# Optimization experiments

Measured on AMD Instinct MI355X. Metric: run time of the kernel, lower is better.

## Reference

```python
import jax, jax.numpy as jnp
import numpy as np

L = 6      # n_latents (hardcoded 6 in original zeros((1,1,6)))
H = 64     # hidden_dim
V = 51     # queue_len + 1
N = 300000 # number of agents/observations
K = 64     # neighbors per slot (flattened c_group)
EPS = 1e-8


def swish(x):
    return x * jax.nn.sigmoid(x)


def encode(obs, We1, be1, We2, be2, We3, be3):
    # obs: [N, 2] -> mu, logvar each [N, 2, L]
    h = swish(obs @ We1 + be1)
    h = swish(h @ We2 + be2)
    out = h @ We3 + be3  # [N, 4L]
    mu, logvar = out[:, :2 * L], out[:, 2 * L:]
    n = obs.shape[0]
    return mu.reshape(n, 2, L), logvar.reshape(n, 2, L)


def decode(z, Wd1, bd1, Wd2, bd2, Wd3, bd3):
    # z: [..., L] -> [..., V]
    h = swish(z @ Wd1 + bd1)
    h = swish(h @ Wd2 + bd2)
    return h @ Wd3 + bd3


def poe(mu_e, lv_e, axis):
    # product of experts along `axis` (ProductOfExperts.forward)
    T = 1.0 / (jnp.exp(lv_e) + EPS)
    sT = jnp.sum(T, axis=axis)
    pd_mu = jnp.sum(mu_e * T, axis=axis) / sT
    pd_logvar = jnp.log(1.0 / sT)
    return pd_mu, pd_logvar


def setup_inputs() -> dict:
    key = jax.random.key(0)
    ks = jax.random.split(key, 12)
    glorot = jax.nn.initializers.glorot_uniform()
    return {
        "obs": jax.random.normal(ks[0], (N, 2), jnp.float32),
        "p": jax.random.uniform(ks[1], (N, 1), jnp.float32),
        "eps_skip": jax.random.normal(ks[2], (N, 2, L), jnp.float32),
        "eps_poe": jax.random.normal(ks[3], (N, 2, L), jnp.float32),
        "neighbor_sched": jax.random.randint(ks[4], (N, 2, K), 0, N, jnp.int32),
        "neighbor_obs": jax.random.randint(ks[5], (N, 2, K), 0, 2, jnp.int32),
        # MessageEncoder params
        "We1": glorot(ks[6], (2, H)), "be1": jnp.zeros((H,), jnp.float32),
        "We2": glorot(ks[7], (H, H)), "be2": jnp.zeros((H,), jnp.float32),
        "We3": glorot(ks[8], (H, 4 * L)), "be3": jnp.zeros((4 * L,), jnp.float32),
        # MessageDecoder params
        "Wd1": glorot(ks[9], (L, H)), "bd1": jnp.zeros((H,), jnp.float32),
        "Wd2": glorot(ks[10], (H, H)), "bd2": jnp.zeros((H,), jnp.float32),
        "Wd3": glorot(ks[11], (H, V)), "bd3": jnp.zeros((V,), jnp.float32),
    }


def reference(obs, p, eps_skip, eps_poe, neighbor_sched, neighbor_obs,
              We1, be1, We2, be2, We3, be3,
              Wd1, bd1, Wd2, bd2, Wd3, bd3):
    n = obs.shape[0]
    mu, logvar = encode(obs, We1, be1, We2, be2, We3, be3)  # [N,2,L]

    # gather neighbor experts: _mus[id_sched][:, id_obs, :]
    nb_mu = mu[neighbor_sched, neighbor_obs]      # [N,2,K,L]
    nb_lv = logvar[neighbor_sched, neighbor_obs]  # [N,2,K,L]

    # experts = [prior N(0,1), own slot, K neighbors] along axis 2
    prior = jnp.zeros((n, 2, 1, L), mu.dtype)  # mu=0, logvar=log(1)=0
    mu_e = jnp.concatenate([prior, mu[:, :, None, :], nb_mu], axis=2)
    lv_e = jnp.concatenate([prior, logvar[:, :, None, :], nb_lv], axis=2)
    pd_mu, pd_lv = poe(mu_e, lv_e, axis=2)  # [N,2,L]

    # reparametrize (training=True)
    z_poe = pd_mu + eps_poe * jnp.exp(0.5 * pd_lv)
    z_skip = mu + eps_skip * jnp.exp(0.5 * logvar)

    rec_poe = decode(z_poe, Wd1, bd1, Wd2, bd2, Wd3, bd3)   # [N,2,V]
    rec_skip = decode(z_skip, Wd1, bd1, Wd2, bd2, Wd3, bd3) # [N,2,V]

    skip = (p[:, 0] < 0.5)[:, None]  # [N,1] -> p[i][0]<0.5 branch
    mus = jnp.where(skip, mu.reshape(n, -1), pd_mu.reshape(n, -1))        # [N,2L]
    logvars = jnp.where(skip, logvar.reshape(n, -1), pd_lv.reshape(n, -1))
    recs = jnp.where(skip, rec_skip.reshape(n, -1), rec_poe.reshape(n, -1))  # [N,2V]
    return recs, mus, logvars
```

## Files before the change

kernel.cpp:

```cpp
#include <hip/hip_runtime.h>
#include <hip/hip_bf16.h>


typedef unsigned short u16;
typedef __hip_bfloat16 bf16;

__device__ __forceinline__ float blo(unsigned int x) {
    union { unsigned int i; float f; } v; v.i = x << 16; return v.f;
}
__device__ __forceinline__ float bhi(unsigned int x) {
    union { unsigned int i; float f; } v; v.i = x & 0xffff0000u; return v.f;
}
__device__ __forceinline__ u16 f2b16(float f) {
    __hip_bfloat16 h = __float2bfloat16(f);
    u16 u; __builtin_memcpy(&u, &h, 2); return u;
}
__device__ __forceinline__ float b2f(u16 u) {
    union { unsigned int i; float f; } v; v.i = ((unsigned int)u) << 16; return v.f;
}
__device__ __forceinline__ float swishf(float x) {
    return x / (1.0f + __expf(-x));
}
__device__ __forceinline__ float ldv(const void* p, size_t i, int isb) {
    return isb ? __bfloat162float(((const bf16*)p)[i]) : ((const float*)p)[i];
}
__device__ __forceinline__ void stv(void* p, size_t i, int isb, float v) {
    if (isb) ((bf16*)p)[i] = __float2bfloat16(v);
    else     ((float*)p)[i] = v;
}

__global__ void k_detect(const unsigned int* __restrict__ obsw, int* __restrict__ flag) {
    unsigned int w = obsw[threadIdx.x];
    unsigned int e = (w >> 7) & 0xFFu;
    bool sane = (e >= 0x70u && e <= 0x87u);
    unsigned long long m = __ballot(sane);
    if (threadIdx.x == 0) flag[0] = (__popcll(m) >= 40) ? 1 : 0;
}

__global__ __launch_bounds__(256) void k_encode(
    const void* __restrict__ obs,
    const void* __restrict__ We1, const void* __restrict__ be1,
    const void* __restrict__ We2, const void* __restrict__ be2,
    const void* __restrict__ We3, const void* __restrict__ be3,
    const int* __restrict__ flag, u16* __restrict__ gt, int N)
{
    __shared__ float sW1[2 * 64];
    __shared__ float sb1[64];
    __shared__ float sW2[64 * 64];
    __shared__ float sb2[64];
    __shared__ float sW3[64 * 24];
    __shared__ float sb3[24];
    __shared__ u16 sh1[64 * 256];
    const int isb = flag[0];
    const int tid = threadIdx.x;
    for (int i = tid; i < 128; i += 256) sW1[i] = ldv(We1, i, isb);
    if (tid < 64) sb1[tid] = ldv(be1, tid, isb);
    for (int i = tid; i < 4096; i += 256) sW2[i] = ldv(We2, i, isb);
    if (tid < 64) sb2[tid] = ldv(be2, tid, isb);
    for (int i = tid; i < 1536; i += 256) sW3[i] = ldv(We3, i, isb);
    if (tid < 24) sb3[tid] = ldv(be3, tid, isb);
    __syncthreads();

    const int n = blockIdx.x * 256 + tid;
    if (n >= N) return;

    const float o0 = ldv(obs, 2 * (size_t)n, isb);
    const float o1 = ldv(obs, 2 * (size_t)n + 1, isb);

#pragma unroll 8
    for (int j = 0; j < 64; ++j) {
        float v = swishf(o0 * sW1[j] + o1 * sW1[64 + j] + sb1[j]);
        sh1[j * 256 + tid] = f2b16(v);
    }

    float o[24];
#pragma unroll
    for (int v = 0; v < 24; ++v) o[v] = sb3[v];

    for (int jc = 0; jc < 4; ++jc) {
        float acc[16];
#pragma unroll
        for (int k = 0; k < 16; ++k) acc[k] = sb2[jc * 16 + k];
        for (int i = 0; i < 64; ++i) {
            const float a = b2f(sh1[i * 256 + tid]);
            const float4* w4 = (const float4*)(sW2 + i * 64 + jc * 16);
#pragma unroll
            for (int k4 = 0; k4 < 4; ++k4) {
                float4 w = w4[k4];
                acc[4 * k4 + 0] += a * w.x; acc[4 * k4 + 1] += a * w.y;
                acc[4 * k4 + 2] += a * w.z; acc[4 * k4 + 3] += a * w.w;
            }
        }
#pragma unroll
        for (int k = 0; k < 16; ++k) {
            const float a = swishf(acc[k]);
            const float4* w4 = (const float4*)(sW3 + (jc * 16 + k) * 24);
#pragma unroll
            for (int v4 = 0; v4 < 6; ++v4) {
                float4 w = w4[v4];
                o[4 * v4 + 0] += a * w.x; o[4 * v4 + 1] += a * w.y;
                o[4 * v4 + 2] += a * w.z; o[4 * v4 + 3] += a * w.w;
            }
        }
    }

    u16* g = gt + (size_t)n * 32;
#pragma unroll
    for (int mod = 0; mod < 2; ++mod) {
        float e[16];
#pragma unroll
        for (int l = 0; l < 6; ++l) {
            e[l]     = o[mod * 6 + l];
            e[6 + l] = o[12 + mod * 6 + l];
        }
        e[12] = 0.f; e[13] = 0.f; e[14] = 0.f; e[15] = 0.f;
        unsigned int pk[8];
#pragma unroll
        for (int i = 0; i < 8; ++i)
            pk[i] = (unsigned int)f2b16(e[2 * i]) | ((unsigned int)f2b16(e[2 * i + 1]) << 16);
        *(int4*)(g + mod * 16)     = make_int4(pk[0], pk[1], pk[2], pk[3]);
        *(int4*)(g + mod * 16 + 8) = make_int4(pk[4], pk[5], pk[6], pk[7]);
    }
}

__global__ __launch_bounds__(256) void k_poe_decode(
    const void* __restrict__ p,
    const void* __restrict__ eps_skip, const void* __restrict__ eps_poe,
    const int* __restrict__ nbs, const int* __restrict__ nbo,
    const void* __restrict__ Wd1, const void* __restrict__ bd1,
    const void* __restrict__ Wd2, const void* __restrict__ bd2,
    const void* __restrict__ Wd3, const void* __restrict__ bd3,
    const int* __restrict__ flag, const u16* __restrict__ gt,
    void* __restrict__ out, int N)
{
    __shared__ float sW1[6 * 64];
    __shared__ float sb1[64];
    __shared__ float sW2[64 * 64];
    __shared__ float sb2[64];
    __shared__ float sW3[64 * 52];
    __shared__ float sb3[52];
    __shared__ u16 sh1[64 * 256];
    const int isb = flag[0];
    const int tid = threadIdx.x;
    for (int i = tid; i < 384; i += 256) sW1[i] = ldv(Wd1, i, isb);
    if (tid < 64) sb1[tid] = ldv(bd1, tid, isb);
    for (int i = tid; i < 4096; i += 256) sW2[i] = ldv(Wd2, i, isb);
    if (tid < 64) sb2[tid] = ldv(bd2, tid, isb);
    for (int t = tid; t < 64 * 52; t += 256) {
        int i = t / 52, v = t - i * 52;
        sW3[t] = (v < 51) ? ldv(Wd3, i * 51 + v, isb) : 0.f;
    }
    if (tid < 52) sb3[tid] = (tid < 51) ? ldv(bd3, tid, isb) : 0.f;
    __syncthreads();

    const int idx = blockIdx.x * 256 + tid;
    const int n = idx >> 1;
    const int mod = idx & 1;
    if (n >= N) return;

    const bool skip = ldv(p, n, isb) < 0.5f;

    const u16* g = gt + (size_t)n * 32 + mod * 16;
    int4 sa = *(const int4*)g;
    int2 sbv = *(const int2*)(g + 8);
    float mu[6], lv[6];
    mu[0] = blo(sa.x); mu[1] = bhi(sa.x); mu[2] = blo(sa.y);
    mu[3] = bhi(sa.y); mu[4] = blo(sa.z); mu[5] = bhi(sa.z);
    lv[0] = blo(sa.w); lv[1] = bhi(sa.w); lv[2] = blo(sbv.x);
    lv[3] = bhi(sbv.x); lv[4] = blo(sbv.y); lv[5] = bhi(sbv.y);

    float z[6], outmu[6], outlv[6];

    if (!skip) {
        float sT[6], sM[6];
        const float priorT = 1.0f / (1.0f + 1e-8f);
#pragma unroll
        for (int l = 0; l < 6; ++l) {
            float T = 1.0f / (__expf(lv[l]) + 1e-8f);
            sT[l] = priorT + T;
            sM[l] = mu[l] * T;
        }
        const int4* ps = (const int4*)(nbs + (size_t)idx * 64);
        const int4* po = (const int4*)(nbo + (size_t)idx * 64);
#pragma unroll 4
        for (int k4 = 0; k4 < 16; ++k4) {
            int4 s4 = ps[k4];
            int4 o4 = po[k4];
            int ss[4] = { s4.x, s4.y, s4.z, s4.w };
            int oo[4] = { o4.x, o4.y, o4.z, o4.w };
#pragma unroll
            for (int u = 0; u < 4; ++u) {
                int sidx = ss[u]; if ((unsigned)sidx >= (unsigned)N) sidx = 0;
                int oidx = oo[u] & 1;
                const u16* e = gt + (size_t)sidx * 32 + oidx * 16;
                int4 a = *(const int4*)e;
                int2 b = *(const int2*)(e + 8);
                float m0 = blo(a.x), m1 = bhi(a.x), m2 = blo(a.y);
                float m3 = bhi(a.y), m4 = blo(a.z), m5 = bhi(a.z);
                float v0 = blo(a.w), v1 = bhi(a.w), v2 = blo(b.x);
                float v3 = bhi(b.x), v4 = blo(b.y), v5 = bhi(b.y);
                float T0 = 1.0f / (__expf(v0) + 1e-8f); sT[0] += T0; sM[0] += m0 * T0;
                float T1 = 1.0f / (__expf(v1) + 1e-8f); sT[1] += T1; sM[1] += m1 * T1;
                float T2 = 1.0f / (__expf(v2) + 1e-8f); sT[2] += T2; sM[2] += m2 * T2;
                float T3 = 1.0f / (__expf(v3) + 1e-8f); sT[3] += T3; sM[3] += m3 * T3;
                float T4 = 1.0f / (__expf(v4) + 1e-8f); sT[4] += T4; sM[4] += m4 * T4;
                float T5 = 1.0f / (__expf(v5) + 1e-8f); sT[5] += T5; sM[5] += m5 * T5;
            }
        }
#pragma unroll
        for (int l = 0; l < 6; ++l) {
            float pm = sM[l] / sT[l];
            outmu[l] = pm;
            outlv[l] = -__logf(sT[l]);
            z[l] = pm + ldv(eps_poe, (size_t)idx * 6 + l, isb) * rsqrtf(sT[l]);
        }
    } else {
#pragma unroll
        for (int l = 0; l < 6; ++l) {
            outmu[l] = mu[l];
            outlv[l] = lv[l];
            z[l] = mu[l] + ldv(eps_skip, (size_t)idx * 6 + l, isb) * __expf(0.5f * lv[l]);
        }
    }

    {
        const size_t om = (size_t)N * 102 + (size_t)idx * 6;
        const size_t ol = (size_t)N * 114 + (size_t)idx * 6;
#pragma unroll
        for (int l = 0; l < 6; ++l) {
            stv(out, om + l, isb, outmu[l]);
            stv(out, ol + l, isb, outlv[l]);
        }
    }

#pragma unroll 4
    for (int j4 = 0; j4 < 16; ++j4) {
        float a0 = sb1[4 * j4 + 0], a1 = sb1[4 * j4 + 1];
        float a2 = sb1[4 * j4 + 2], a3 = sb1[4 * j4 + 3];
#pragma unroll
        for (int l = 0; l < 6; ++l) {
            float4 w = ((const float4*)(sW1 + l * 64))[j4];
            a0 += z[l] * w.x; a1 += z[l] * w.y;
            a2 += z[l] * w.z; a3 += z[l] * w.w;
        }
        sh1[(4 * j4 + 0) * 256 + tid] = f2b16(swishf(a0));
        sh1[(4 * j4 + 1) * 256 + tid] = f2b16(swishf(a1));
        sh1[(4 * j4 + 2) * 256 + tid] = f2b16(swishf(a2));
        sh1[(4 * j4 + 3) * 256 + tid] = f2b16(swishf(a3));
    }

    float r[52];
#pragma unroll
    for (int v = 0; v < 52; ++v) r[v] = sb3[v];

    for (int jc = 0; jc < 4; ++jc) {
        float acc[16];
#pragma unroll
        for (int k = 0; k < 16; ++k) acc[k] = sb2[jc * 16 + k];
        for (int i = 0; i < 64; ++i) {
            const float a = b2f(sh1[i * 256 + tid]);
            const float4* w4 = (const float4*)(sW2 + i * 64 + jc * 16);
#pragma unroll
            for (int k4 = 0; k4 < 4; ++k4) {
                float4 w = w4[k4];
                acc[4 * k4 + 0] += a * w.x; acc[4 * k4 + 1] += a * w.y;
                acc[4 * k4 + 2] += a * w.z; acc[4 * k4 + 3] += a * w.w;
            }
        }
#pragma unroll
        for (int k = 0; k < 16; ++k) {
            const float a = swishf(acc[k]);
            const float4* w4 = (const float4*)(sW3 + (jc * 16 + k) * 52);
#pragma unroll
            for (int v4 = 0; v4 < 13; ++v4) {
                float4 w = w4[v4];
                r[4 * v4 + 0] += a * w.x; r[4 * v4 + 1] += a * w.y;
                r[4 * v4 + 2] += a * w.z; r[4 * v4 + 3] += a * w.w;
            }
        }
    }

    const size_t ro = (size_t)n * 102 + (size_t)mod * 51;
#pragma unroll
    for (int v = 0; v < 51; ++v) stv(out, ro + v, isb, r[v]);
}

extern "C" void kernel_launch(void* const* d_in, const int* in_sizes, int n_in,
                              void* d_out, int out_size, void* d_ws, size_t ws_size,
                              hipStream_t stream) {
    const int N = in_sizes[0] / 2;
    const void* obs      = d_in[0];
    const void* p        = d_in[1];
    const void* eps_skip = d_in[2];
    const void* eps_poe  = d_in[3];
    const int*  nbs      = (const int*)d_in[4];
    const int*  nbo      = (const int*)d_in[5];

    int* flag = (int*)d_ws;
    u16* gt   = (u16*)d_ws + 32;

    dim3 blk(256);
    dim3 grdA((N + 255) / 256);
    dim3 grdB((2 * N + 255) / 256);
    hipLaunchKernelGGL(k_detect, dim3(1), dim3(64), 0, stream,
                       (const unsigned int*)obs, flag);
    hipLaunchKernelGGL(k_encode, grdA, blk, 0, stream,
                       obs, d_in[6], d_in[7], d_in[8], d_in[9], d_in[10], d_in[11],
                       flag, gt, N);
    hipLaunchKernelGGL(k_poe_decode, grdB, blk, 0, stream,
                       p, eps_skip, eps_poe, nbs, nbo,
                       d_in[12], d_in[13], d_in[14], d_in[15], d_in[16], d_in[17],
                       flag, gt, (void*)d_out, N);
}
```

Measured before the change: 1.263 ms.

## Split PoE gather from decode MLP, keep hidden activations in registers

The fused PoE+decode kernel is split in two. A lightweight gather kernel (launch bounds 256,4, no shared memory) writes the sampled latents z to a workspace buffer, and a separate decode kernel reads them back. Both the encoder and decoder drop the 32KB per-block shared hidden-activation buffer and keep packed bf16 activations in registers with a fully unrolled inner loop. Nontemporal loads and stores are added for streaming inputs and outputs. The aim is higher occupancy so the latency-bound random gather is better hidden. The cost is an extra launch, a z round-trip through global memory, and more register pressure in the MLP kernels.

Result: slower. 2.318 ms (+83.5%).

```diff
diff --git a/kernel.cpp b/kernel.cpp
--- a/kernel.cpp
+++ b/kernel.cpp
@@ -4,6 +4,7 @@
 
 typedef unsigned short u16;
 typedef __hip_bfloat16 bf16;
+typedef int iv4 __attribute__((ext_vector_type(4)));
 
 __device__ __forceinline__ float blo(unsigned int x) {
     union { unsigned int i; float f; } v; v.i = x << 16; return v.f;
@@ -27,6 +28,14 @@
 __device__ __forceinline__ void stv(void* p, size_t i, int isb, float v) {
     if (isb) ((bf16*)p)[i] = __float2bfloat16(v);
     else     ((float*)p)[i] = v;
+}
+__device__ __forceinline__ float ldv_nt(const void* p, size_t i, int isb) {
+    if (isb) return b2f(__builtin_nontemporal_load((const u16*)p + i));
+    return __builtin_nontemporal_load((const float*)p + i);
+}
+__device__ __forceinline__ void stv_nt(void* p, size_t i, int isb, float v) {
+    if (isb) { u16 b = f2b16(v); __builtin_nontemporal_store(b, (u16*)p + i); }
+    else     __builtin_nontemporal_store(v, (float*)p + i);
 }
 
 __global__ void k_detect(const unsigned int* __restrict__ obsw, int* __restrict__ flag) {
@@ -50,7 +59,6 @@
     __shared__ float sb2[64];
     __shared__ float sW3[64 * 24];
     __shared__ float sb3[24];
-    __shared__ u16 sh1[64 * 256];
     const int isb = flag[0];
     const int tid = threadIdx.x;
     for (int i = tid; i < 128; i += 256) sW1[i] = ldv(We1, i, isb);
@@ -64,13 +72,15 @@
     const int n = blockIdx.x * 256 + tid;
     if (n >= N) return;
 
-    const float o0 = ldv(obs, 2 * (size_t)n, isb);
-    const float o1 = ldv(obs, 2 * (size_t)n + 1, isb);
-
-#pragma unroll 8
-    for (int j = 0; j < 64; ++j) {
-        float v = swishf(o0 * sW1[j] + o1 * sW1[64 + j] + sb1[j]);
-        sh1[j * 256 + tid] = f2b16(v);
+    const float o0 = ldv_nt(obs, 2 * (size_t)n, isb);
+    const float o1 = ldv_nt(obs, 2 * (size_t)n + 1, isb);
+
+    unsigned int hp[32];
+#pragma unroll
+    for (int j2 = 0; j2 < 32; ++j2) {
+        float v0 = swishf(o0 * sW1[2 * j2]     + o1 * sW1[64 + 2 * j2]     + sb1[2 * j2]);
+        float v1 = swishf(o0 * sW1[2 * j2 + 1] + o1 * sW1[64 + 2 * j2 + 1] + sb1[2 * j2 + 1]);
+        hp[j2] = (unsigned int)f2b16(v0) | ((unsigned int)f2b16(v1) << 16);
     }
 
     float o[24];
@@ -81,14 +91,16 @@
         float acc[16];
 #pragma unroll
         for (int k = 0; k < 16; ++k) acc[k] = sb2[jc * 16 + k];
+#pragma unroll
         for (int i = 0; i < 64; ++i) {
-            const float a = b2f(sh1[i * 256 + tid]);
+            const unsigned int w = hp[i >> 1];
+            const float a = (i & 1) ? bhi(w) : blo(w);
             const float4* w4 = (const float4*)(sW2 + i * 64 + jc * 16);
 #pragma unroll
             for (int k4 = 0; k4 < 4; ++k4) {
-                float4 w = w4[k4];
-                acc[4 * k4 + 0] += a * w.x; acc[4 * k4 + 1] += a * w.y;
-                acc[4 * k4 + 2] += a * w.z; acc[4 * k4 + 3] += a * w.w;
+                float4 ww = w4[k4];
+                acc[4 * k4 + 0] += a * ww.x; acc[4 * k4 + 1] += a * ww.y;
+                acc[4 * k4 + 2] += a * ww.z; acc[4 * k4 + 3] += a * ww.w;
             }
         }
 #pragma unroll
@@ -123,42 +135,20 @@
     }
 }
 
-__global__ __launch_bounds__(256) void k_poe_decode(
+__global__ __launch_bounds__(256, 4) void k_poe(
     const void* __restrict__ p,
     const void* __restrict__ eps_skip, const void* __restrict__ eps_poe,
     const int* __restrict__ nbs, const int* __restrict__ nbo,
-    const void* __restrict__ Wd1, const void* __restrict__ bd1,
-    const void* __restrict__ Wd2, const void* __restrict__ bd2,
-    const void* __restrict__ Wd3, const void* __restrict__ bd3,
     const int* __restrict__ flag, const u16* __restrict__ gt,
-    void* __restrict__ out, int N)
+    float* __restrict__ zbuf, void* __restrict__ out, int N)
 {
-    __shared__ float sW1[6 * 64];
-    __shared__ float sb1[64];
-    __shared__ float sW2[64 * 64];
-    __shared__ float sb2[64];
-    __shared__ float sW3[64 * 52];
-    __shared__ float sb3[52];
-    __shared__ u16 sh1[64 * 256];
     const int isb = flag[0];
-    const int tid = threadIdx.x;
-    for (int i = tid; i < 384; i += 256) sW1[i] = ldv(Wd1, i, isb);
-    if (tid < 64) sb1[tid] = ldv(bd1, tid, isb);
-    for (int i = tid; i < 4096; i += 256) sW2[i] = ldv(Wd2, i, isb);
-    if (tid < 64) sb2[tid] = ldv(bd2, tid, isb);
-    for (int t = tid; t < 64 * 52; t += 256) {
-        int i = t / 52, v = t - i * 52;
-        sW3[t] = (v < 51) ? ldv(Wd3, i * 51 + v, isb) : 0.f;
-    }
-    if (tid < 52) sb3[tid] = (tid < 51) ? ldv(bd3, tid, isb) : 0.f;
-    __syncthreads();
-
-    const int idx = blockIdx.x * 256 + tid;
+    const int idx = blockIdx.x * 256 + threadIdx.x;
     const int n = idx >> 1;
     const int mod = idx & 1;
     if (n >= N) return;
 
-    const bool skip = ldv(p, n, isb) < 0.5f;
+    const bool skip = ldv_nt(p, n, isb) < 0.5f;
 
     const u16* g = gt + (size_t)n * 32 + mod * 16;
     int4 sa = *(const int4*)g;
@@ -180,14 +170,14 @@
             sT[l] = priorT + T;
             sM[l] = mu[l] * T;
         }
-        const int4* ps = (const int4*)(nbs + (size_t)idx * 64);
-        const int4* po = (const int4*)(nbo + (size_t)idx * 64);
+        const iv4* ps = (const iv4*)(nbs + (size_t)idx * 64);
+        const iv4* po = (const iv4*)(nbo + (size_t)idx * 64);
 #pragma unroll 4
         for (int k4 = 0; k4 < 16; ++k4) {
-            int4 s4 = ps[k4];
-            int4 o4 = po[k4];
-            int ss[4] = { s4.x, s4.y, s4.z, s4.w };
-            int oo[4] = { o4.x, o4.y, o4.z, o4.w };
+            iv4 s4 = __builtin_nontemporal_load(ps + k4);
+            iv4 o4 = __builtin_nontemporal_load(po + k4);
+            int ss[4] = { s4[0], s4[1], s4[2], s4[3] };
+            int oo[4] = { o4[0], o4[1], o4[2], o4[3] };
 #pragma unroll
             for (int u = 0; u < 4; ++u) {
                 int sidx = ss[u]; if ((unsigned)sidx >= (unsigned)N) sidx = 0;
@@ -212,28 +202,66 @@
             float pm = sM[l] / sT[l];
             outmu[l] = pm;
             outlv[l] = -__logf(sT[l]);
-            z[l] = pm + ldv(eps_poe, (size_t)idx * 6 + l, isb) * rsqrtf(sT[l]);
+            z[l] = pm + ldv_nt(eps_poe, (size_t)idx * 6 + l, isb) * rsqrtf(sT[l]);
         }
     } else {
 #pragma unroll
         for (int l = 0; l < 6; ++l) {
             outmu[l] = mu[l];
             outlv[l] = lv[l];
-            z[l] = mu[l] + ldv(eps_skip, (size_t)idx * 6 + l, isb) * __expf(0.5f * lv[l]);
-        }
-    }
-
-    {
-        const size_t om = (size_t)N * 102 + (size_t)idx * 6;
-        const size_t ol = (size_t)N * 114 + (size_t)idx * 6;
-#pragma unroll
-        for (int l = 0; l < 6; ++l) {
-            stv(out, om + l, isb, outmu[l]);
-            stv(out, ol + l, isb, outlv[l]);
-        }
-    }
-
-#pragma unroll 4
+            z[l] = mu[l] + ldv_nt(eps_skip, (size_t)idx * 6 + l, isb) * __expf(0.5f * lv[l]);
+        }
+    }
+
+#pragma unroll
+    for (int l = 0; l < 6; ++l) zbuf[(size_t)idx * 6 + l] = z[l];
+
+    const size_t om = (size_t)N * 102 + (size_t)idx * 6;
+    const size_t ol = (size_t)N * 114 + (size_t)idx * 6;
+#pragma unroll
+    for (int l = 0; l < 6; ++l) {
+        stv_nt(out, om + l, isb, outmu[l]);
+        stv_nt(out, ol + l, isb, outlv[l]);
+    }
+}
+
+__global__ __launch_bounds__(256) void k_decode(
+    const void* __restrict__ Wd1, const void* __restrict__ bd1,
+    const void* __restrict__ Wd2, const void* __restrict__ bd2,
+    const void* __restrict__ Wd3, const void* __restrict__ bd3,
+    const int* __restrict__ flag, const float* __restrict__ zbuf,
+    void* __restrict__ out, int N)
+{
+    __shared__ float sW1[6 * 64];
+    __shared__ float sb1[64];
+    __shared__ float sW2[64 * 64];
+    __shared__ float sb2[64];
+    __shared__ float sW3[64 * 52];
+    __shared__ float sb3[52];
+    const int isb = flag[0];
+    const int tid = threadIdx.x;
+    for (int i = tid; i < 384; i += 256) sW1[i] = ldv(Wd1, i, isb);
+    if (tid < 64) sb1[tid] = ldv(bd1, tid, isb);
+    for (int i = tid; i < 4096; i += 256) sW2[i] = ldv(Wd2, i, isb);
+    if (tid < 64) sb2[tid] = ldv(bd2, tid, isb);
+    for (int t = tid; t < 64 * 52; t += 256) {
+        int i = t / 52, v = t - i * 52;
+        sW3[t] = (v < 51) ? ldv(Wd3, i * 51 + v, isb) : 0.f;
+    }
+    if (tid < 52) sb3[tid] = (tid < 51) ? ldv(bd3, tid, isb) : 0.f;
+    __syncthreads();
+
+    const int idx = blockIdx.x * 256 + tid;
+    const int n = idx >> 1;
+    const int mod = idx & 1;
+    if (n >= N) return;
+
+    float z[6];
+#pragma unroll
+    for (int l = 0; l < 6; ++l) z[l] = zbuf[(size_t)idx * 6 + l];
+
+    unsigned int hp[32];
+#pragma unroll
     for (int j4 = 0; j4 < 16; ++j4) {
         float a0 = sb1[4 * j4 + 0], a1 = sb1[4 * j4 + 1];
         float a2 = sb1[4 * j4 + 2], a3 = sb1[4 * j4 + 3];
@@ -243,10 +271,8 @@
             a0 += z[l] * w.x; a1 += z[l] * w.y;
             a2 += z[l] * w.z; a3 += z[l] * w.w;
         }
-        sh1[(4 * j4 + 0) * 256 + tid] = f2b16(swishf(a0));
-        sh1[(4 * j4 + 1) * 256 + tid] = f2b16(swishf(a1));
-        sh1[(4 * j4 + 2) * 256 + tid] = f2b16(swishf(a2));
-        sh1[(4 * j4 + 3) * 256 + tid] = f2b16(swishf(a3));
+        hp[2 * j4]     = (unsigned int)f2b16(swishf(a0)) | ((unsigned int)f2b16(swishf(a1)) << 16);
+        hp[2 * j4 + 1] = (unsigned int)f2b16(swishf(a2)) | ((unsigned int)f2b16(swishf(a3)) << 16);
     }
 
     float r[52];
@@ -257,14 +283,16 @@
         float acc[16];
 #pragma unroll
         for (int k = 0; k < 16; ++k) acc[k] = sb2[jc * 16 + k];
+#pragma unroll
         for (int i = 0; i < 64; ++i) {
-            const float a = b2f(sh1[i * 256 + tid]);
+            const unsigned int w = hp[i >> 1];
+            const float a = (i & 1) ? bhi(w) : blo(w);
             const float4* w4 = (const float4*)(sW2 + i * 64 + jc * 16);
 #pragma unroll
             for (int k4 = 0; k4 < 4; ++k4) {
-                float4 w = w4[k4];
-                acc[4 * k4 + 0] += a * w.x; acc[4 * k4 + 1] += a * w.y;
-                acc[4 * k4 + 2] += a * w.z; acc[4 * k4 + 3] += a * w.w;
+                float4 ww = w4[k4];
+                acc[4 * k4 + 0] += a * ww.x; acc[4 * k4 + 1] += a * ww.y;
+                acc[4 * k4 + 2] += a * ww.z; acc[4 * k4 + 3] += a * ww.w;
             }
         }
 #pragma unroll
@@ -282,7 +310,7 @@
 
     const size_t ro = (size_t)n * 102 + (size_t)mod * 51;
 #pragma unroll
-    for (int v = 0; v < 51; ++v) stv(out, ro + v, isb, r[v]);
+    for (int v = 0; v < 51; ++v) stv_nt(out, ro + v, isb, r[v]);
 }
 
 extern "C" void kernel_launch(void* const* d_in, const int* in_sizes, int n_in,
@@ -298,6 +326,7 @@
 
     int* flag = (int*)d_ws;
     u16* gt   = (u16*)d_ws + 32;
+    float* zbuf = (float*)((char*)d_ws + 64 + (size_t)N * 64);
 
     dim3 blk(256);
     dim3 grdA((N + 255) / 256);
@@ -307,8 +336,10 @@
     hipLaunchKernelGGL(k_encode, grdA, blk, 0, stream,
                        obs, d_in[6], d_in[7], d_in[8], d_in[9], d_in[10], d_in[11],
                        flag, gt, N);
-    hipLaunchKernelGGL(k_poe_decode, grdB, blk, 0, stream,
+    hipLaunchKernelGGL(k_poe, grdB, blk, 0, stream,
                        p, eps_skip, eps_poe, nbs, nbo,
+                       flag, gt, zbuf, (void*)d_out, N);
+    hipLaunchKernelGGL(k_decode, grdB, blk, 0, stream,
                        d_in[12], d_in[13], d_in[14], d_in[15], d_in[16], d_in[17],
-                       flag, gt, (void*)d_out, N);
-}
+                       flag, zbuf, (void*)d_out, N);
+}
```
